# Performance work log

Measured on AMD Instinct MI355X. Metric: run time of the kernel, lower is better.

## Reference

```python
import jax, jax.numpy as jnp
import numpy as np

N = 8192  # n_nodes
E = 262144  # edges per adjacency (avg degree 32)


def setup_inputs() -> dict:
    key = jax.random.key(0)
    k0, k1, k2, k3, k4, k5 = jax.random.split(key, 6)
    rows_s = jax.random.randint(k0, (E,), 0, N)
    cols_s = jax.random.randint(k1, (E,), 0, N)
    vals_s = jax.random.uniform(k2, (E,), dtype=jnp.float32)
    rows_t = jax.random.randint(k3, (E,), 0, N)
    cols_t = jax.random.randint(k4, (E,), 0, N)
    vals_t = jax.random.uniform(k5, (E,), dtype=jnp.float32)
    gamma = jnp.zeros((1,), dtype=jnp.float32)  # learnable scalar, init 0.0
    return {
        "rows_s": rows_s, "cols_s": cols_s, "vals_s": vals_s,
        "rows_t": rows_t, "cols_t": cols_t, "vals_t": vals_t,
        "gamma": gamma,
    }


def reference(rows_s, cols_s, vals_s, rows_t, cols_t, vals_t, gamma):
    # coalesce + to_dense: scatter-add duplicates into dense [N, N]
    As = jnp.zeros((N, N), dtype=vals_s.dtype).at[rows_s, cols_s].add(vals_s)
    At = jnp.zeros((N, N), dtype=vals_t.dtype).at[rows_t, cols_t].add(vals_t)
    alpha = jax.nn.sigmoid(gamma[0])
    Af = alpha * As + (1.0 - alpha) * At
    row_sum = jnp.sum(Af, axis=1, keepdims=True)  # [N, 1]
    row_sum = jnp.where(row_sum == 0, jnp.ones_like(row_sum), row_sum)
    Af = Af / row_sum
    # torch returns Af.to_sparse(); dense Af is the equivalent value-complete output
    return Af
```

## Files before the change

kernel.cpp:

```cpp
#include <hip/hip_runtime.h>
#include <math.h>

#define NN 8192
#define NE 262144
#define TOTAL (2*NE)
#define CAP 128
#define HALF 4096

typedef float f4 __attribute__((ext_vector_type(4)));

struct Pair { int c; float v; };

#define BK_OFF (65536)
#define OV_OFF (65536 + (size_t)NN * CAP * 8)

__global__ __launch_bounds__(256) void fill_kernel(
        const int* __restrict__ rows_s, const int* __restrict__ cols_s,
        const float* __restrict__ vals_s,
        const int* __restrict__ rows_t, const int* __restrict__ cols_t,
        const float* __restrict__ vals_t,
        const float* __restrict__ gamma,
        int* __restrict__ cnt, Pair* __restrict__ bucket,
        int* __restrict__ ovf_cnt, int4* __restrict__ ovf) {
    int i = blockIdx.x * blockDim.x + threadIdx.x;
    float alpha = 1.0f / (1.0f + expf(-gamma[0]));
    int r, c; float v, w;
    if (i < NE) { r = rows_s[i]; c = cols_s[i]; v = vals_s[i]; w = alpha; }
    else { int j = i - NE; r = rows_t[j]; c = cols_t[j]; v = vals_t[j]; w = 1.0f - alpha; }
    float wv = w * v;
    int pos = atomicAdd(&cnt[r], 1);
    if (pos < CAP) {
        Pair p; p.c = c; p.v = wv;
        bucket[r * CAP + pos] = p;
    } else {
        int k = atomicAdd(ovf_cnt, 1);
        int4 e; e.x = r; e.y = c; e.z = __float_as_int(wv); e.w = 0;
        ovf[k] = e;
    }
}

__global__ __launch_bounds__(256) void row_kernel(
        const int* __restrict__ cnt, const Pair* __restrict__ bucket,
        const int* __restrict__ ovf_cnt, const int4* __restrict__ ovf,
        float* __restrict__ out) {
    __shared__ float row[HALF];
    __shared__ float red[4];
    int r    = blockIdx.x >> 1;
    int cbase = (blockIdx.x & 1) * HALF;
    int t = threadIdx.x;

    f4* row4 = (f4*)row;
    #pragma unroll
    for (int k = t; k < HALF / 4; k += 256) { f4 z = {0.f, 0.f, 0.f, 0.f}; row4[k] = z; }
    int n = cnt[r];
    int nb = n < CAP ? n : CAP;
    __syncthreads();

    float part = 0.0f;
    for (int k = t; k < nb; k += 256) {
        Pair p = bucket[r * CAP + k];
        part += p.v;
        int lc = p.c - cbase;
        if ((unsigned)lc < HALF) atomicAdd(&row[lc], p.v);
    }
    int no = *ovf_cnt;
    if (no > 0) {
        for (int k = t; k < no; k += 256) {
            int4 e = ovf[k];
            if (e.x == r) {
                float v = __int_as_float(e.z);
                part += v;
                int lc = e.y - cbase;
                if ((unsigned)lc < HALF) atomicAdd(&row[lc], v);
            }
        }
    }

    #pragma unroll
    for (int o = 32; o > 0; o >>= 1) part += __shfl_down(part, o, 64);
    if ((t & 63) == 0) red[t >> 6] = part;
    __syncthreads();
    float total = red[0] + red[1] + red[2] + red[3];
    float inv = (total == 0.0f) ? 1.0f : 1.0f / total;

    f4* out4 = (f4*)(out + (size_t)r * NN + cbase);
    #pragma unroll
    for (int k = t; k < HALF / 4; k += 256) {
        f4 x = row4[k];
        x *= inv;
        __builtin_nontemporal_store(x, &out4[k]);
    }
}

extern "C" void kernel_launch(void* const* d_in, const int* in_sizes, int n_in,
                              void* d_out, int out_size, void* d_ws, size_t ws_size,
                              hipStream_t stream) {
    const int*   rows_s = (const int*)  d_in[0];
    const int*   cols_s = (const int*)  d_in[1];
    const float* vals_s = (const float*)d_in[2];
    const int*   rows_t = (const int*)  d_in[3];
    const int*   cols_t = (const int*)  d_in[4];
    const float* vals_t = (const float*)d_in[5];
    const float* gamma  = (const float*)d_in[6];

    float* out     = (float*)d_out;
    char*  ws      = (char*)d_ws;
    int*   cnt     = (int*)ws;
    int*   ovf_cnt = (int*)(ws + 32768);
    Pair*  bucket  = (Pair*)(ws + BK_OFF);
    int4*  ovf     = (int4*)(ws + OV_OFF);

    (void)hipMemsetAsync(ws, 0, 32772, stream);

    fill_kernel<<<TOTAL / 256, 256, 0, stream>>>(rows_s, cols_s, vals_s,
                                                 rows_t, cols_t, vals_t,
                                                 gamma, cnt, bucket, ovf_cnt, ovf);
    row_kernel<<<2 * NN, 256, 0, stream>>>(cnt, bucket, ovf_cnt, ovf, out);
}
```

Before: 310.5 us.

## Bucket edges per row half and precompute row sums with atomics in fill

The fill kernel now buckets edges by row and column half (SCAP 64 per segment) and accumulates row sums with global float atomics. Each row_kernel block therefore reads only its own segment's entries, where before both half-row blocks scanned the full row bucket. The change also swaps nontemporal output stores for plain stores. The cost is more global atomics in fill, and with smaller segment capacity the linear overflow scan is more likely to be triggered.

```diff
diff --git a/kernel.cpp b/kernel.cpp
--- a/kernel.cpp
+++ b/kernel.cpp
@@ -4,15 +4,18 @@
 #define NN 8192
 #define NE 262144
 #define TOTAL (2*NE)
-#define CAP 128
+#define NSEG 2
 #define HALF 4096
+#define SCAP 64
 
 typedef float f4 __attribute__((ext_vector_type(4)));
 
 struct Pair { int c; float v; };
 
-#define BK_OFF (65536)
-#define OV_OFF (65536 + (size_t)NN * CAP * 8)
+#define RS_OFF  65536
+#define OC_OFF  98304
+#define BK_OFF  131072
+#define OV_OFF  (131072 + (size_t)NN * NSEG * SCAP * 8)
 
 __global__ __launch_bounds__(256) void fill_kernel(
         const int* __restrict__ rows_s, const int* __restrict__ cols_s,
@@ -20,7 +23,8 @@
         const int* __restrict__ rows_t, const int* __restrict__ cols_t,
         const float* __restrict__ vals_t,
         const float* __restrict__ gamma,
-        int* __restrict__ cnt, Pair* __restrict__ bucket,
+        int* __restrict__ cnt, float* __restrict__ rowsum,
+        Pair* __restrict__ bucket,
         int* __restrict__ ovf_cnt, int4* __restrict__ ovf) {
     int i = blockIdx.x * blockDim.x + threadIdx.x;
     float alpha = 1.0f / (1.0f + expf(-gamma[0]));
@@ -28,10 +32,12 @@
     if (i < NE) { r = rows_s[i]; c = cols_s[i]; v = vals_s[i]; w = alpha; }
     else { int j = i - NE; r = rows_t[j]; c = cols_t[j]; v = vals_t[j]; w = 1.0f - alpha; }
     float wv = w * v;
-    int pos = atomicAdd(&cnt[r], 1);
-    if (pos < CAP) {
-        Pair p; p.c = c; p.v = wv;
-        bucket[r * CAP + pos] = p;
+    atomicAdd(&rowsum[r], wv);
+    int b = r * NSEG + (c >> 12);
+    int pos = atomicAdd(&cnt[b], 1);
+    if (pos < SCAP) {
+        Pair p; p.c = c & (HALF - 1); p.v = wv;
+        bucket[b * SCAP + pos] = p;
     } else {
         int k = atomicAdd(ovf_cnt, 1);
         int4 e; e.x = r; e.y = c; e.z = __float_as_int(wv); e.w = 0;
@@ -40,55 +46,45 @@
 }
 
 __global__ __launch_bounds__(256) void row_kernel(
-        const int* __restrict__ cnt, const Pair* __restrict__ bucket,
+        const int* __restrict__ cnt, const float* __restrict__ rowsum,
+        const Pair* __restrict__ bucket,
         const int* __restrict__ ovf_cnt, const int4* __restrict__ ovf,
         float* __restrict__ out) {
     __shared__ float row[HALF];
-    __shared__ float red[4];
-    int r    = blockIdx.x >> 1;
-    int cbase = (blockIdx.x & 1) * HALF;
-    int t = threadIdx.x;
+    int b   = blockIdx.x;
+    int r   = b >> 1;
+    int seg = b & 1;
+    int t   = threadIdx.x;
 
     f4* row4 = (f4*)row;
     #pragma unroll
     for (int k = t; k < HALF / 4; k += 256) { f4 z = {0.f, 0.f, 0.f, 0.f}; row4[k] = z; }
-    int n = cnt[r];
-    int nb = n < CAP ? n : CAP;
+    int n  = cnt[b];
+    int nb = n < SCAP ? n : SCAP;
+    float rs = rowsum[r];
     __syncthreads();
 
-    float part = 0.0f;
     for (int k = t; k < nb; k += 256) {
-        Pair p = bucket[r * CAP + k];
-        part += p.v;
-        int lc = p.c - cbase;
-        if ((unsigned)lc < HALF) atomicAdd(&row[lc], p.v);
+        Pair p = bucket[b * SCAP + k];
+        atomicAdd(&row[p.c], p.v);
     }
     int no = *ovf_cnt;
     if (no > 0) {
         for (int k = t; k < no; k += 256) {
             int4 e = ovf[k];
-            if (e.x == r) {
-                float v = __int_as_float(e.z);
-                part += v;
-                int lc = e.y - cbase;
-                if ((unsigned)lc < HALF) atomicAdd(&row[lc], v);
-            }
+            if (e.x == r && (e.y >> 12) == seg)
+                atomicAdd(&row[e.y & (HALF - 1)], __int_as_float(e.z));
         }
     }
+    __syncthreads();
 
-    #pragma unroll
-    for (int o = 32; o > 0; o >>= 1) part += __shfl_down(part, o, 64);
-    if ((t & 63) == 0) red[t >> 6] = part;
-    __syncthreads();
-    float total = red[0] + red[1] + red[2] + red[3];
-    float inv = (total == 0.0f) ? 1.0f : 1.0f / total;
-
-    f4* out4 = (f4*)(out + (size_t)r * NN + cbase);
+    float inv = (rs == 0.0f) ? 1.0f : 1.0f / rs;
+    f4* out4 = (f4*)(out + (size_t)r * NN + seg * HALF);
     #pragma unroll
     for (int k = t; k < HALF / 4; k += 256) {
         f4 x = row4[k];
         x *= inv;
-        __builtin_nontemporal_store(x, &out4[k]);
+        out4[k] = x;
     }
 }
 
@@ -106,14 +102,17 @@
     float* out     = (float*)d_out;
     char*  ws      = (char*)d_ws;
     int*   cnt     = (int*)ws;
-    int*   ovf_cnt = (int*)(ws + 32768);
+    float* rowsum  = (float*)(ws + RS_OFF);
+    int*   ovf_cnt = (int*)(ws + OC_OFF);
     Pair*  bucket  = (Pair*)(ws + BK_OFF);
     int4*  ovf     = (int4*)(ws + OV_OFF);
 
-    (void)hipMemsetAsync(ws, 0, 32772, stream);
+    (void)hipMemsetAsync(ws, 0, OC_OFF + 4, stream);
 
     fill_kernel<<<TOTAL / 256, 256, 0, stream>>>(rows_s, cols_s, vals_s,
                                                  rows_t, cols_t, vals_t,
-                                                 gamma, cnt, bucket, ovf_cnt, ovf);
-    row_kernel<<<2 * NN, 256, 0, stream>>>(cnt, bucket, ovf_cnt, ovf, out);
+                                                 gamma, cnt, rowsum, bucket,
+                                                 ovf_cnt, ovf);
+    row_kernel<<<NN * NSEG, 256, 0, stream>>>(cnt, rowsum, bucket,
+                                              ovf_cnt, ovf, out);
 }
```

New measurement: 336.0 us. 1.08x slower.
